# Performance work log

Hardware: AMD Instinct MI355X
Metric: run time of the kernel (lower is better)

## Reference

```python
import jax, jax.numpy as jnp
import numpy as np

H = 2048          # hidden_size
E = 8             # num_experts
TOPK = 2          # num_experts_per_tok
I = 1408          # moe_intermediate_size
IS = 5632         # shared_expert_intermediate_size


def setup_inputs() -> dict:
    key = jax.random.key(0)
    ks = jax.random.split(key, 10)
    s = 0.02
    return {
        "hidden_states": jax.random.normal(ks[0], (2, 512, H), dtype=jnp.float32),
        "gate_w": jax.random.normal(ks[1], (H, E), dtype=jnp.float32) * s,
        "wg": jax.random.normal(ks[2], (E, H, I), dtype=jnp.float32) * s,
        "wu": jax.random.normal(ks[3], (E, H, I), dtype=jnp.float32) * s,
        "wd": jax.random.normal(ks[4], (E, I, H), dtype=jnp.float32) * s,
        "sg": jax.random.normal(ks[5], (H, IS), dtype=jnp.float32) * s,
        "su": jax.random.normal(ks[6], (H, IS), dtype=jnp.float32) * s,
        "sd": jax.random.normal(ks[7], (IS, H), dtype=jnp.float32) * s,
        "shared_gate_w": jax.random.normal(ks[8], (H, 1), dtype=jnp.float32) * s,
    }


def reference(hidden_states, gate_w, wg, wu, wd, sg, su, sd, shared_gate_w):
    B, S, Hd = hidden_states.shape
    x = hidden_states.reshape(-1, Hd)                       # [T, H]
    # Router (softmax in fp32, as in the torch code)
    router_logits = x @ gate_w                              # [T, E]
    probs = jax.nn.softmax(router_logits.astype(jnp.float32), axis=-1)
    rw, sel = jax.lax.top_k(probs, TOPK)                    # [T, K]
    # norm_topk_prob = False -> no renormalization
    rw = rw.astype(x.dtype)
    # Dense combine weights: w[t,e] = sum_k rw[t,k] * 1[sel[t,k]==e]
    combine = (jax.nn.one_hot(sel, E, dtype=x.dtype) * rw[..., None]).sum(axis=1)  # [T, E]
    # Per-expert SwiGLU MLP over all tokens, zero-weighted where unselected
    g = jnp.einsum('th,ehi->eti', x, wg)                    # [E, T, I]
    u = jnp.einsum('th,ehi->eti', x, wu)                    # [E, T, I]
    y = jnp.einsum('eti,eih->eth', jax.nn.silu(g) * u, wd)  # [E, T, H]
    moe_out = jnp.einsum('eth,te->th', y, combine)          # [T, H]
    # Shared expert with sigmoid gate
    shared = (jax.nn.silu(x @ sg) * (x @ su)) @ sd          # [T, H]
    shared = jax.nn.sigmoid(x @ shared_gate_w) * shared     # [T, H]
    final = moe_out + shared
    return final.reshape(B, S, Hd), router_logits
```

## Files before the change

### kernel.cpp

```cpp
#include <hip/hip_runtime.h>
#include <cstdint>
#include <cstddef>

#define Tn 1024
#define Hn 2048
#define En 8
#define In 1408
#define ISn 5632

typedef __attribute__((ext_vector_type(8))) short bf16x8;
typedef __attribute__((ext_vector_type(4))) float f32x4;

__device__ __forceinline__ unsigned short f2bf(float f) {
  unsigned u = __builtin_bit_cast(unsigned, f);
  u += 0x7fffu + ((u >> 16) & 1u);
  return (unsigned short)(u >> 16);
}

#define PK2(a, b) ((unsigned)f2bf(a) | ((unsigned)f2bf(b) << 16))
#define SWZC(row, kc) (((kc) ^ ((row) & 7) ^ (((row) >> 3) & 7)) & 7)
#define SWZ(row, bir) (((row) << 7) | (SWZC((row), ((bir) >> 4)) << 4) | ((bir) & 15))

__global__ void router_kernel(const float* __restrict__ x, const float* __restrict__ gw,
                              const float* __restrict__ sgw, float* __restrict__ logits_out,
                              float* __restrict__ sgate, int* __restrict__ tokList,
                              float* __restrict__ wgt, int* __restrict__ cnt) {
  int t = blockIdx.x;
  int l = threadIdx.x;
  const float* xr = x + (size_t)t * Hn;
  float acc[En];
#pragma unroll
  for (int e = 0; e < En; ++e) acc[e] = 0.f;
  float accs = 0.f;
  for (int h = l; h < Hn; h += 64) {
    float xv = xr[h];
    const float4 g0 = *(const float4*)(gw + (size_t)h * En);
    const float4 g1 = *(const float4*)(gw + (size_t)h * En + 4);
    acc[0] += xv * g0.x; acc[1] += xv * g0.y; acc[2] += xv * g0.z; acc[3] += xv * g0.w;
    acc[4] += xv * g1.x; acc[5] += xv * g1.y; acc[6] += xv * g1.z; acc[7] += xv * g1.w;
    accs += xv * sgw[h];
  }
#pragma unroll
  for (int e = 0; e < En; ++e) {
#pragma unroll
    for (int off = 32; off > 0; off >>= 1) acc[e] += __shfl_down(acc[e], off);
  }
#pragma unroll
  for (int off = 32; off > 0; off >>= 1) accs += __shfl_down(accs, off);
  if (l == 0) {
    float mx = acc[0];
#pragma unroll
    for (int e = 1; e < En; ++e) mx = fmaxf(mx, acc[e]);
    float p[En], s = 0.f;
#pragma unroll
    for (int e = 0; e < En; ++e) { p[e] = expf(acc[e] - mx); s += p[e]; }
    float inv = 1.f / s;
#pragma unroll
    for (int e = 0; e < En; ++e) p[e] *= inv;
    int i1 = 0;
#pragma unroll
    for (int e = 1; e < En; ++e) if (p[e] > p[i1]) i1 = e;
    int i2 = (i1 == 0) ? 1 : 0;
#pragma unroll
    for (int e = 0; e < En; ++e) if (e != i1 && p[e] > p[i2]) i2 = e;
    int p1 = atomicAdd(&cnt[i1], 1);
    tokList[(i1 << 10) + p1] = t; wgt[(i1 << 10) + p1] = p[i1];
    int p2 = atomicAdd(&cnt[i2], 1);
    tokList[(i2 << 10) + p2] = t; wgt[(i2 << 10) + p2] = p[i2];
    sgate[t] = 1.f / (1.f + expf(-accs));
#pragma unroll
    for (int e = 0; e < En; ++e) logits_out[t * En + e] = acc[e];
  }
}

__global__ void cvt_x_kernel(const float* __restrict__ x, unsigned short* __restrict__ xb) {
  int i = (blockIdx.x * 256 + threadIdx.x) << 2;
  float4 v = *(const float4*)(x + i);
  ushort4 o;
  o.x = f2bf(v.x); o.y = f2bf(v.y); o.z = f2bf(v.z); o.w = f2bf(v.w);
  *(ushort4*)(xb + i) = o;
}

__device__ __forceinline__ void stage_b(char* sB, const float* __restrict__ src, int ldb, int tid) {
  const int kb = tid >> 5;
  const int nb = tid & 31;
  const float* p = src + (size_t)(kb * 8) * ldb + nb * 4;
  float4 r0 = *(const float4*)p; p += ldb;
  float4 r1 = *(const float4*)p; p += ldb;
  float4 r2 = *(const float4*)p; p += ldb;
  float4 r3 = *(const float4*)p; p += ldb;
  float4 r4 = *(const float4*)p; p += ldb;
  float4 r5 = *(const float4*)p; p += ldb;
  float4 r6 = *(const float4*)p; p += ldb;
  float4 r7 = *(const float4*)p;
  uint4 pk;
  int n, off;
#define STORE_ROW(J, F)                                                        \
  n = nb * 4 + (J);                                                            \
  pk.x = PK2(r0.F, r1.F); pk.y = PK2(r2.F, r3.F);                              \
  pk.z = PK2(r4.F, r5.F); pk.w = PK2(r6.F, r7.F);                              \
  off = (n << 7) | (SWZC(n, kb) << 4);                                         \
  *(uint4*)(sB + off) = pk;
  STORE_ROW(0, x)
  STORE_ROW(1, y)
  STORE_ROW(2, z)
  STORE_ROW(3, w)
#undef STORE_ROW
}

__global__ __launch_bounds__(256, 2)
void gateup_kernel(const unsigned short* __restrict__ xb,
                   const float* __restrict__ Wg, const float* __restrict__ Wu,
                   const float* __restrict__ wgt, const float* __restrict__ sgate,
                   const int* __restrict__ tokList, const int* __restrict__ cnt,
                   unsigned short* __restrict__ actout, int N, int mode) {
  const int e = blockIdx.y;
  const int nt = blockIdx.x >> 3, mt = blockIdx.x & 7;
  const int cntE = (mode == 0) ? cnt[e] : Tn;
  const int m0 = mt << 7, n0 = nt << 7;
  if (m0 >= cntE) return;

  __shared__ char smem[48 * 1024];
  char* sA = smem;
  char* sBg = smem + 16 * 1024;
  char* sBu = smem + 32 * 1024;

  const int tid = threadIdx.x;
  const int lane = tid & 63;
  const int wid = tid >> 6;
  const int wm = wid >> 1, wn = wid & 1;

  const float* Bg0 = Wg + (size_t)e * Hn * N + n0;
  const float* Bu0 = Wu + (size_t)e * Hn * N + n0;
  unsigned short* aout = actout + (size_t)e * Tn * N;

  int tokq[4];
#pragma unroll
  for (int q = 0; q < 4; ++q) {
    int row = (tid + (q << 8)) >> 3;
    int m = m0 + row;
    if (mode == 0) {
      int mc = m < cntE ? m : cntE - 1;
      tokq[q] = tokList[(e << 10) + mc];
    } else {
      tokq[q] = m;
    }
  }

  f32x4 accg[4][4], accu[4][4];
#pragma unroll
  for (int i = 0; i < 4; ++i)
#pragma unroll
    for (int j = 0; j < 4; ++j) {
      accg[i][j] = {0.f, 0.f, 0.f, 0.f};
      accu[i][j] = {0.f, 0.f, 0.f, 0.f};
    }

  for (int kt = 0; kt < Hn / 64; ++kt) {
    const int k0 = kt << 6;
#pragma unroll
    for (int q = 0; q < 4; ++q) {
      int cc = tid + (q << 8);
      int row = cc >> 3, c = cc & 7;
      uint4 v = *(const uint4*)(xb + (size_t)tokq[q] * Hn + k0 + (c << 3));
      *(uint4*)(sA + SWZ(row, c << 4)) = v;
    }
    stage_b(sBg, Bg0 + (size_t)k0 * N, N, tid);
    stage_b(sBu, Bu0 + (size_t)k0 * N, N, tid);
    __syncthreads();
#pragma unroll
    for (int kk = 0; kk < 2; ++kk) {
      bf16x8 af[4], bg[4], bu[4];
      const int bir = (kk << 6) + ((lane >> 4) << 4);
#pragma unroll
      for (int mi = 0; mi < 4; ++mi) {
        int row = (wm << 6) + (mi << 4) + (lane & 15);
        af[mi] = *(const bf16x8*)(sA + SWZ(row, bir));
      }
#pragma unroll
      for (int ni = 0; ni < 4; ++ni) {
        int n = (wn << 6) + (ni << 4) + (lane & 15);
        bg[ni] = *(const bf16x8*)(sBg + SWZ(n, bir));
        bu[ni] = *(const bf16x8*)(sBu + SWZ(n, bir));
      }
#pragma unroll
      for (int mi = 0; mi < 4; ++mi)
#pragma unroll
        for (int ni = 0; ni < 4; ++ni) {
          accg[mi][ni] = __builtin_amdgcn_mfma_f32_16x16x32_bf16(af[mi], bg[ni], accg[mi][ni], 0, 0, 0);
          accu[mi][ni] = __builtin_amdgcn_mfma_f32_16x16x32_bf16(af[mi], bu[ni], accu[mi][ni], 0, 0, 0);
        }
    }
    __syncthreads();
  }

#pragma unroll
  for (int mi = 0; mi < 4; ++mi)
#pragma unroll
    for (int ni = 0; ni < 4; ++ni)
#pragma unroll
      for (int r = 0; r < 4; ++r) {
        int m = m0 + (wm << 6) + (mi << 4) + ((lane >> 4) << 2) + r;
        int n = n0 + (wn << 6) + (ni << 4) + (lane & 15);
        if (m < cntE) {
          float sc = (mode == 0) ? wgt[(e << 10) + m] : sgate[m];
          float g = accg[mi][ni][r];
          float u = accu[mi][ni][r];
          aout[(size_t)m * N + n] = f2bf(sc * (g / (1.f + __expf(-g))) * u);
        }
      }
}

__global__ __launch_bounds__(256, 2)
void down_e_kernel(const unsigned short* __restrict__ act, const float* __restrict__ wd,
                   const int* __restrict__ tokList, const int* __restrict__ cnt,
                   float* __restrict__ out) {
  const int e = blockIdx.y;
  const int nt = blockIdx.x >> 3, mt = blockIdx.x & 7;
  const int cntE = cnt[e];
  const int m0 = mt << 7, n0 = nt << 7;
  if (m0 >= cntE) return;

  __shared__ char smem[32 * 1024];
  char* sA = smem;
  char* sB = smem + 16 * 1024;

  const int tid = threadIdx.x;
  const int lane = tid & 63;
  const int wid = tid >> 6;
  const int wm = wid >> 1, wn = wid & 1;

  const unsigned short* aBase = act + ((size_t)e * Tn + m0) * In;
  const float* bBase = wd + (size_t)e * In * Hn + n0;

  f32x4 acc[4][4];
#pragma unroll
  for (int i = 0; i < 4; ++i)
#pragma unroll
    for (int j = 0; j < 4; ++j) acc[i][j] = {0.f, 0.f, 0.f, 0.f};

  for (int kt = 0; kt < In / 64; ++kt) {
    const int k0 = kt << 6;
#pragma unroll
    for (int q = 0; q < 4; ++q) {
      int cc = tid + (q << 8);
      int row = cc >> 3, c = cc & 7;
      uint4 v = *(const uint4*)(aBase + (size_t)row * In + k0 + (c << 3));
      *(uint4*)(sA + SWZ(row, c << 4)) = v;
    }
    stage_b(sB, bBase + (size_t)k0 * Hn, Hn, tid);
    __syncthreads();
#pragma unroll
    for (int kk = 0; kk < 2; ++kk) {
      bf16x8 af[4], bf[4];
      const int bir = (kk << 6) + ((lane >> 4) << 4);
#pragma unroll
      for (int mi = 0; mi < 4; ++mi) {
        int row = (wm << 6) + (mi << 4) + (lane & 15);
        af[mi] = *(const bf16x8*)(sA + SWZ(row, bir));
      }
#pragma unroll
      for (int ni = 0; ni < 4; ++ni) {
        int n = (wn << 6) + (ni << 4) + (lane & 15);
        bf[ni] = *(const bf16x8*)(sB + SWZ(n, bir));
      }
#pragma unroll
      for (int mi = 0; mi < 4; ++mi)
#pragma unroll
        for (int ni = 0; ni < 4; ++ni)
          acc[mi][ni] = __builtin_amdgcn_mfma_f32_16x16x32_bf16(af[mi], bf[ni], acc[mi][ni], 0, 0, 0);
    }
    __syncthreads();
  }

#pragma unroll
  for (int mi = 0; mi < 4; ++mi)
#pragma unroll
    for (int ni = 0; ni < 4; ++ni)
#pragma unroll
      for (int r = 0; r < 4; ++r) {
        int m = m0 + (wm << 6) + (mi << 4) + ((lane >> 4) << 2) + r;
        int n = n0 + (wn << 6) + (ni << 4) + (lane & 15);
        if (m < cntE) {
          int tok = tokList[(e << 10) + m];
          atomicAdd(out + (size_t)tok * Hn + n, acc[mi][ni][r]);
        }
      }
}

__global__ __launch_bounds__(256, 2)
void down_s_kernel(const unsigned short* __restrict__ acts, const float* __restrict__ sd,
                   float* __restrict__ out) {
  const int nt = blockIdx.x >> 3, mt = blockIdx.x & 7;
  const int m0 = mt << 7, n0 = nt << 7;
  const int ktBeg = blockIdx.y * 44, ktEnd = ktBeg + 44;

  __shared__ char smem[32 * 1024];
  char* sA = smem;
  char* sB = smem + 16 * 1024;

  const int tid = threadIdx.x;
  const int lane = tid & 63;
  const int wid = tid >> 6;
  const int wm = wid >> 1, wn = wid & 1;

  f32x4 acc[4][4];
#pragma unroll
  for (int i = 0; i < 4; ++i)
#pragma unroll
    for (int j = 0; j < 4; ++j) acc[i][j] = {0.f, 0.f, 0.f, 0.f};

  for (int kt = ktBeg; kt < ktEnd; ++kt) {
    const int k0 = kt << 6;
#pragma unroll
    for (int q = 0; q < 4; ++q) {
      int cc = tid + (q << 8);
      int row = cc >> 3, c = cc & 7;
      uint4 v = *(const uint4*)(acts + (size_t)(m0 + row) * ISn + k0 + (c << 3));
      *(uint4*)(sA + SWZ(row, c << 4)) = v;
    }
    stage_b(sB, sd + (size_t)k0 * Hn + n0, Hn, tid);
    __syncthreads();
#pragma unroll
    for (int kk = 0; kk < 2; ++kk) {
      bf16x8 af[4], bf[4];
      const int bir = (kk << 6) + ((lane >> 4) << 4);
#pragma unroll
      for (int mi = 0; mi < 4; ++mi) {
        int row = (wm << 6) + (mi << 4) + (lane & 15);
        af[mi] = *(const bf16x8*)(sA + SWZ(row, bir));
      }
#pragma unroll
      for (int ni = 0; ni < 4; ++ni) {
        int n = (wn << 6) + (ni << 4) + (lane & 15);
        bf[ni] = *(const bf16x8*)(sB + SWZ(n, bir));
      }
#pragma unroll
      for (int mi = 0; mi < 4; ++mi)
#pragma unroll
        for (int ni = 0; ni < 4; ++ni)
          acc[mi][ni] = __builtin_amdgcn_mfma_f32_16x16x32_bf16(af[mi], bf[ni], acc[mi][ni], 0, 0, 0);
    }
    __syncthreads();
  }

#pragma unroll
  for (int mi = 0; mi < 4; ++mi)
#pragma unroll
    for (int ni = 0; ni < 4; ++ni)
#pragma unroll
      for (int r = 0; r < 4; ++r) {
        int m = m0 + (wm << 6) + (mi << 4) + ((lane >> 4) << 2) + r;
        int n = n0 + (wn << 6) + (ni << 4) + (lane & 15);
        atomicAdd(out + (size_t)m * Hn + n, acc[mi][ni][r]);
      }
}

extern "C" void kernel_launch(void* const* d_in, const int* in_sizes, int n_in,
                              void* d_out, int out_size, void* d_ws, size_t ws_size,
                              hipStream_t stream) {
  const float* x   = (const float*)d_in[0];
  const float* gw  = (const float*)d_in[1];
  const float* wg  = (const float*)d_in[2];
  const float* wu  = (const float*)d_in[3];
  const float* wd  = (const float*)d_in[4];
  const float* sg  = (const float*)d_in[5];
  const float* su  = (const float*)d_in[6];
  const float* sd  = (const float*)d_in[7];
  const float* sgw = (const float*)d_in[8];
  float* out = (float*)d_out;
  float* logits_out = out + (size_t)Tn * Hn;

  char* w = (char*)d_ws;
  int*   cnt     = (int*)w;
  float* sgate   = (float*)(w + 4096);
  int*   tokList = (int*)(w + 8192);
  float* wgt     = (float*)(w + 40960);
  unsigned short* xb   = (unsigned short*)(w + 131072);
  unsigned short* actE = xb + (size_t)Tn * Hn;
  unsigned short* actS = actE + (size_t)En * Tn * In;

  hipMemsetAsync(d_out, 0, (size_t)out_size * sizeof(float), stream);
  hipMemsetAsync(cnt, 0, En * sizeof(int), stream);
  router_kernel<<<Tn, 64, 0, stream>>>(x, gw, sgw, logits_out, sgate, tokList, wgt, cnt);
  cvt_x_kernel<<<(Tn * Hn / 4) / 256, 256, 0, stream>>>(x, xb);
  gateup_kernel<<<dim3((In / 128) * 8, En), 256, 0, stream>>>(xb, wg, wu, wgt, sgate, tokList, cnt, actE, In, 0);
  gateup_kernel<<<dim3((ISn / 128) * 8, 1), 256, 0, stream>>>(xb, sg, su, wgt, sgate, tokList, cnt, actS, ISn, 1);
  down_e_kernel<<<dim3(16 * 8, En), 256, 0, stream>>>(actE, wd, tokList, cnt, out);
  down_s_kernel<<<dim3(16 * 8, 2), 256, 0, stream>>>(actS, sd, out);
}
```

Measured before the change: 904.3 us.

## Pre-transpose weights to bf16 and stage GEMM tiles via direct global-to-LDS loads

Adds a prepass kernel that converts and transposes all expert and shared weights to bf16 K-contiguous layout every call. The GEMM kernels then fill LDS with global_load_lds 16-byte copies in swizzled order instead of loading fp32, converting, and repacking in registers. Gate/up and down launches for routed and shared experts are merged into single launches. This removes in-loop conversion and uncoalesced strided fp32 reads, but adds a full read-and-write pass over all weights each call.

```diff
diff --git a/kernel.cpp b/kernel.cpp
--- a/kernel.cpp
+++ b/kernel.cpp
@@ -11,13 +11,16 @@
 typedef __attribute__((ext_vector_type(8))) short bf16x8;
 typedef __attribute__((ext_vector_type(4))) float f32x4;
 
+typedef __attribute__((address_space(3))) unsigned int lds_u32_t;
+typedef __attribute__((address_space(1))) const unsigned int gbl_u32_t;
+#define GLL16(gp, lp) __builtin_amdgcn_global_load_lds((gbl_u32_t*)(gp), (lds_u32_t*)(lp), 16, 0, 0)
+
 __device__ __forceinline__ unsigned short f2bf(float f) {
   unsigned u = __builtin_bit_cast(unsigned, f);
   u += 0x7fffu + ((u >> 16) & 1u);
   return (unsigned short)(u >> 16);
 }
 
-#define PK2(a, b) ((unsigned)f2bf(a) | ((unsigned)f2bf(b) << 16))
 #define SWZC(row, kc) (((kc) ^ ((row) & 7) ^ (((row) >> 3) & 7)) & 7)
 #define SWZ(row, bir) (((row) << 7) | (SWZC((row), ((bir) >> 4)) << 4) | ((bir) & 15))
 
@@ -81,42 +84,80 @@
   *(ushort4*)(xb + i) = o;
 }
 
-__device__ __forceinline__ void stage_b(char* sB, const float* __restrict__ src, int ldb, int tid) {
-  const int kb = tid >> 5;
-  const int nb = tid & 31;
-  const float* p = src + (size_t)(kb * 8) * ldb + nb * 4;
-  float4 r0 = *(const float4*)p; p += ldb;
-  float4 r1 = *(const float4*)p; p += ldb;
-  float4 r2 = *(const float4*)p; p += ldb;
-  float4 r3 = *(const float4*)p; p += ldb;
-  float4 r4 = *(const float4*)p; p += ldb;
-  float4 r5 = *(const float4*)p; p += ldb;
-  float4 r6 = *(const float4*)p; p += ldb;
-  float4 r7 = *(const float4*)p;
-  uint4 pk;
-  int n, off;
-#define STORE_ROW(J, F)                                                        \
-  n = nb * 4 + (J);                                                            \
-  pk.x = PK2(r0.F, r1.F); pk.y = PK2(r2.F, r3.F);                              \
-  pk.z = PK2(r4.F, r5.F); pk.w = PK2(r6.F, r7.F);                              \
-  off = (n << 7) | (SWZC(n, kb) << 4);                                         \
-  *(uint4*)(sB + off) = pk;
-  STORE_ROW(0, x)
-  STORE_ROW(1, y)
-  STORE_ROW(2, z)
-  STORE_ROW(3, w)
-#undef STORE_ROW
+__global__ void trans_cvt_kernel(const float* __restrict__ wg, const float* __restrict__ wu,
+                                 const float* __restrict__ wd, const float* __restrict__ sg,
+                                 const float* __restrict__ su, const float* __restrict__ sd,
+                                 unsigned short* __restrict__ wgT, unsigned short* __restrict__ wuT,
+                                 unsigned short* __restrict__ wdT, unsigned short* __restrict__ sgT,
+                                 unsigned short* __restrict__ suT, unsigned short* __restrict__ sdT) {
+  __shared__ unsigned short lds[64][68];
+  const int bx = blockIdx.x, tid = threadIdx.x;
+  const float* src; unsigned short* dst; int R, C, tr, tc;
+  if (bx < 11264) {
+    int b = (bx < 5632) ? bx : bx - 5632;
+    const float* s0 = (bx < 5632) ? wg : wu;
+    unsigned short* d0 = (bx < 5632) ? wgT : wuT;
+    int e = b / 704, t = b - e * 704;
+    src = s0 + (size_t)e * Hn * In; dst = d0 + (size_t)e * In * Hn;
+    R = Hn; C = In; tr = t / 22; tc = t - tr * 22;
+  } else if (bx < 16896) {
+    int b = bx - 11264; int e = b / 704, t = b - e * 704;
+    src = wd + (size_t)e * In * Hn; dst = wdT + (size_t)e * Hn * In;
+    R = In; C = Hn; tr = t / 32; tc = t - tr * 32;
+  } else if (bx < 22528) {
+    int b = bx - 16896;
+    src = (b < 2816) ? sg : su; dst = (b < 2816) ? sgT : suT;
+    if (b >= 2816) b -= 2816;
+    R = Hn; C = ISn; tr = b / 88; tc = b - tr * 88;
+  } else {
+    int b = bx - 22528;
+    src = sd; dst = sdT; R = ISn; C = Hn; tr = b / 32; tc = b - tr * 32;
+  }
+  const int r0 = tr << 6, c0 = tc << 6;
+#pragma unroll
+  for (int q = 0; q < 4; ++q) {
+    int r = (tid >> 4) + (q << 4);
+    int c = (tid & 15) << 2;
+    float4 v = *(const float4*)(src + (size_t)(r0 + r) * C + c0 + c);
+    ushort4 o; o.x = f2bf(v.x); o.y = f2bf(v.y); o.z = f2bf(v.z); o.w = f2bf(v.w);
+    *(ushort4*)&lds[r][c] = o;
+  }
+  __syncthreads();
+  {
+    int oc = tid >> 2, ch = tid & 3;
+#pragma unroll
+    for (int g = ch; g < 8; g += 4) {
+      unsigned t0, t1, t2, t3;
+      t0 = (unsigned)lds[(g << 3) + 0][oc] | ((unsigned)lds[(g << 3) + 1][oc] << 16);
+      t1 = (unsigned)lds[(g << 3) + 2][oc] | ((unsigned)lds[(g << 3) + 3][oc] << 16);
+      t2 = (unsigned)lds[(g << 3) + 4][oc] | ((unsigned)lds[(g << 3) + 5][oc] << 16);
+      t3 = (unsigned)lds[(g << 3) + 6][oc] | ((unsigned)lds[(g << 3) + 7][oc] << 16);
+      uint4 o; o.x = t0; o.y = t1; o.z = t2; o.w = t3;
+      *(uint4*)(dst + (size_t)(c0 + oc) * R + r0 + (g << 3)) = o;
+    }
+  }
 }
 
 __global__ __launch_bounds__(256, 2)
 void gateup_kernel(const unsigned short* __restrict__ xb,
-                   const float* __restrict__ Wg, const float* __restrict__ Wu,
+                   const unsigned short* __restrict__ wgT, const unsigned short* __restrict__ wuT,
+                   const unsigned short* __restrict__ sgT, const unsigned short* __restrict__ suT,
                    const float* __restrict__ wgt, const float* __restrict__ sgate,
                    const int* __restrict__ tokList, const int* __restrict__ cnt,
-                   unsigned short* __restrict__ actout, int N, int mode) {
-  const int e = blockIdx.y;
-  const int nt = blockIdx.x >> 3, mt = blockIdx.x & 7;
-  const int cntE = (mode == 0) ? cnt[e] : Tn;
+                   unsigned short* __restrict__ actE, unsigned short* __restrict__ actS) {
+  const int bx = blockIdx.x;
+  int e, nt, mt, N, cntE, mode;
+  const unsigned short *bgp, *bup;
+  unsigned short* aout;
+  if (bx < 704) {
+    mode = 0; e = bx / 88; int r = bx - e * 88; nt = r >> 3; mt = r & 7;
+    N = In; cntE = cnt[e];
+    bgp = wgT + (size_t)e * In * Hn; bup = wuT + (size_t)e * In * Hn;
+    aout = actE + (size_t)e * Tn * In;
+  } else {
+    mode = 1; e = 0; int r = bx - 704; nt = r >> 3; mt = r & 7;
+    N = ISn; cntE = Tn; bgp = sgT; bup = suT; aout = actS;
+  }
   const int m0 = mt << 7, n0 = nt << 7;
   if (m0 >= cntE) return;
 
@@ -125,27 +166,26 @@
   char* sBg = smem + 16 * 1024;
   char* sBu = smem + 32 * 1024;
 
-  const int tid = threadIdx.x;
-  const int lane = tid & 63;
-  const int wid = tid >> 6;
+  const int tid = threadIdx.x, lane = tid & 63, wid = tid >> 6;
   const int wm = wid >> 1, wn = wid & 1;
-
-  const float* Bg0 = Wg + (size_t)e * Hn * N + n0;
-  const float* Bu0 = Wu + (size_t)e * Hn * N + n0;
-  unsigned short* aout = actout + (size_t)e * Tn * N;
-
-  int tokq[4];
+  const int qr = lane >> 3;
+  const int qc = lane & 7;
+
+  const char *gA[4], *gB[4], *gU[4];
 #pragma unroll
   for (int q = 0; q < 4; ++q) {
-    int row = (tid + (q << 8)) >> 3;
+    int row = (wid << 5) + (q << 3) + qr;
+    int chunk = SWZC(row, qc);
     int m = m0 + row;
-    if (mode == 0) {
-      int mc = m < cntE ? m : cntE - 1;
-      tokq[q] = tokList[(e << 10) + mc];
-    } else {
-      tokq[q] = m;
-    }
-  }
+    int tok;
+    if (mode == 0) { int mc = m < cntE ? m : cntE - 1; tok = tokList[(e << 10) + mc]; }
+    else tok = m;
+    gA[q] = (const char*)(xb + (size_t)tok * Hn) + chunk * 16;
+    int n = n0 + row;
+    gB[q] = (const char*)(bgp + (size_t)n * Hn) + chunk * 16;
+    gU[q] = (const char*)(bup + (size_t)n * Hn) + chunk * 16;
+  }
+  const int lbase = wid << 12;
 
   f32x4 accg[4][4], accu[4][4];
 #pragma unroll
@@ -157,16 +197,14 @@
     }
 
   for (int kt = 0; kt < Hn / 64; ++kt) {
-    const int k0 = kt << 6;
+    const int koff = kt << 7;
 #pragma unroll
     for (int q = 0; q < 4; ++q) {
-      int cc = tid + (q << 8);
-      int row = cc >> 3, c = cc & 7;
-      uint4 v = *(const uint4*)(xb + (size_t)tokq[q] * Hn + k0 + (c << 3));
-      *(uint4*)(sA + SWZ(row, c << 4)) = v;
-    }
-    stage_b(sBg, Bg0 + (size_t)k0 * N, N, tid);
-    stage_b(sBu, Bu0 + (size_t)k0 * N, N, tid);
+      GLL16(gA[q] + koff, sA + lbase + (q << 10));
+      GLL16(gB[q] + koff, sBg + lbase + (q << 10));
+      GLL16(gU[q] + koff, sBu + lbase + (q << 10));
+    }
+    asm volatile("s_waitcnt vmcnt(0)" ::: "memory");
     __syncthreads();
 #pragma unroll
     for (int kk = 0; kk < 2; ++kk) {
@@ -212,26 +250,46 @@
 }
 
 __global__ __launch_bounds__(256, 2)
-void down_e_kernel(const unsigned short* __restrict__ act, const float* __restrict__ wd,
-                   const int* __restrict__ tokList, const int* __restrict__ cnt,
-                   float* __restrict__ out) {
-  const int e = blockIdx.y;
-  const int nt = blockIdx.x >> 3, mt = blockIdx.x & 7;
-  const int cntE = cnt[e];
+void down_kernel(const unsigned short* __restrict__ actE, const unsigned short* __restrict__ actS,
+                 const unsigned short* __restrict__ wdT, const unsigned short* __restrict__ sdT,
+                 const int* __restrict__ tokList, const int* __restrict__ cnt,
+                 float* __restrict__ out) {
+  const int bx = blockIdx.x;
+  int e, nt, mt, cntE, mode, ktBeg, ktEnd, ldk;
+  const unsigned short *aBase, *bBase;
+  if (bx < 1024) {
+    mode = 0; e = bx >> 7; int r = bx & 127; nt = r >> 3; mt = r & 7;
+    cntE = cnt[e];
+    if ((mt << 7) >= cntE) return;
+    ldk = In; ktBeg = 0; ktEnd = In / 64;
+    aBase = actE + (size_t)e * Tn * In + (size_t)(mt << 7) * In;
+    bBase = wdT + (size_t)e * Hn * In + (size_t)(nt << 7) * In;
+  } else {
+    mode = 1; e = 0; int bs = bx - 1024; int split = bs >> 7; int r = bs & 127;
+    nt = r >> 3; mt = r & 7; cntE = Tn;
+    ldk = ISn; ktBeg = split * 44; ktEnd = ktBeg + 44;
+    aBase = actS + (size_t)(mt << 7) * ISn;
+    bBase = sdT + (size_t)(nt << 7) * ISn;
+  }
   const int m0 = mt << 7, n0 = nt << 7;
-  if (m0 >= cntE) return;
 
   __shared__ char smem[32 * 1024];
   char* sA = smem;
   char* sB = smem + 16 * 1024;
 
-  const int tid = threadIdx.x;
-  const int lane = tid & 63;
-  const int wid = tid >> 6;
+  const int tid = threadIdx.x, lane = tid & 63, wid = tid >> 6;
   const int wm = wid >> 1, wn = wid & 1;
-
-  const unsigned short* aBase = act + ((size_t)e * Tn + m0) * In;
-  const float* bBase = wd + (size_t)e * In * Hn + n0;
+  const int qr = lane >> 3, qc = lane & 7;
+
+  const char *gA[4], *gB[4];
+#pragma unroll
+  for (int q = 0; q < 4; ++q) {
+    int row = (wid << 5) + (q << 3) + qr;
+    int chunk = SWZC(row, qc);
+    gA[q] = (const char*)(aBase + (size_t)row * ldk) + chunk * 16;
+    gB[q] = (const char*)(bBase + (size_t)row * ldk) + chunk * 16;
+  }
+  const int lbase = wid << 12;
 
   f32x4 acc[4][4];
 #pragma unroll
@@ -239,16 +297,14 @@
 #pragma unroll
     for (int j = 0; j < 4; ++j) acc[i][j] = {0.f, 0.f, 0.f, 0.f};
 
-  for (int kt = 0; kt < In / 64; ++kt) {
-    const int k0 = kt << 6;
+  for (int kt = ktBeg; kt < ktEnd; ++kt) {
+    const int koff = kt << 7;
 #pragma unroll
     for (int q = 0; q < 4; ++q) {
-      int cc = tid + (q << 8);
-      int row = cc >> 3, c = cc & 7;
-      uint4 v = *(const uint4*)(aBase + (size_t)row * In + k0 + (c << 3));
-      *(uint4*)(sA + SWZ(row, c << 4)) = v;
-    }
-    stage_b(sB, bBase + (size_t)k0 * Hn, Hn, tid);
+      GLL16(gA[q] + koff, sA + lbase + (q << 10));
+      GLL16(gB[q] + koff, sB + lbase + (q << 10));
+    }
+    asm volatile("s_waitcnt vmcnt(0)" ::: "memory");
     __syncthreads();
 #pragma unroll
     for (int kk = 0; kk < 2; ++kk) {
@@ -281,78 +337,14 @@
       for (int r = 0; r < 4; ++r) {
         int m = m0 + (wm << 6) + (mi << 4) + ((lane >> 4) << 2) + r;
         int n = n0 + (wn << 6) + (ni << 4) + (lane & 15);
-        if (m < cntE) {
-          int tok = tokList[(e << 10) + m];
-          atomicAdd(out + (size_t)tok * Hn + n, acc[mi][ni][r]);
+        if (mode == 0) {
+          if (m < cntE) {
+            int tok = tokList[(e << 10) + m];
+            atomicAdd(out + (size_t)tok * Hn + n, acc[mi][ni][r]);
+          }
+        } else {
+          atomicAdd(out + (size_t)m * Hn + n, acc[mi][ni][r]);
         }
-      }
-}
-
-__global__ __launch_bounds__(256, 2)
-void down_s_kernel(const unsigned short* __restrict__ acts, const float* __restrict__ sd,
-                   float* __restrict__ out) {
-  const int nt = blockIdx.x >> 3, mt = blockIdx.x & 7;
-  const int m0 = mt << 7, n0 = nt << 7;
-  const int ktBeg = blockIdx.y * 44, ktEnd = ktBeg + 44;
-
-  __shared__ char smem[32 * 1024];
-  char* sA = smem;
-  char* sB = smem + 16 * 1024;
-
-  const int tid = threadIdx.x;
-  const int lane = tid & 63;
-  const int wid = tid >> 6;
-  const int wm = wid >> 1, wn = wid & 1;
-
-  f32x4 acc[4][4];
-#pragma unroll
-  for (int i = 0; i < 4; ++i)
-#pragma unroll
-    for (int j = 0; j < 4; ++j) acc[i][j] = {0.f, 0.f, 0.f, 0.f};
-
-  for (int kt = ktBeg; kt < ktEnd; ++kt) {
-    const int k0 = kt << 6;
-#pragma unroll
-    for (int q = 0; q < 4; ++q) {
-      int cc = tid + (q << 8);
-      int row = cc >> 3, c = cc & 7;
-      uint4 v = *(const uint4*)(acts + (size_t)(m0 + row) * ISn + k0 + (c << 3));
-      *(uint4*)(sA + SWZ(row, c << 4)) = v;
-    }
-    stage_b(sB, sd + (size_t)k0 * Hn + n0, Hn, tid);
-    __syncthreads();
-#pragma unroll
-    for (int kk = 0; kk < 2; ++kk) {
-      bf16x8 af[4], bf[4];
-      const int bir = (kk << 6) + ((lane >> 4) << 4);
-#pragma unroll
-      for (int mi = 0; mi < 4; ++mi) {
-        int row = (wm << 6) + (mi << 4) + (lane & 15);
-        af[mi] = *(const bf16x8*)(sA + SWZ(row, bir));
-      }
-#pragma unroll
-      for (int ni = 0; ni < 4; ++ni) {
-        int n = (wn << 6) + (ni << 4) + (lane & 15);
-        bf[ni] = *(const bf16x8*)(sB + SWZ(n, bir));
-      }
-#pragma unroll
-      for (int mi = 0; mi < 4; ++mi)
-#pragma unroll
-        for (int ni = 0; ni < 4; ++ni)
-          acc[mi][ni] = __builtin_amdgcn_mfma_f32_16x16x32_bf16(af[mi], bf[ni], acc[mi][ni], 0, 0, 0);
-    }
-    __syncthreads();
-  }
-
-#pragma unroll
-  for (int mi = 0; mi < 4; ++mi)
-#pragma unroll
-    for (int ni = 0; ni < 4; ++ni)
-#pragma unroll
-      for (int r = 0; r < 4; ++r) {
-        int m = m0 + (wm << 6) + (mi << 4) + ((lane >> 4) << 2) + r;
-        int n = n0 + (wn << 6) + (ni << 4) + (lane & 15);
-        atomicAdd(out + (size_t)m * Hn + n, acc[mi][ni][r]);
       }
 }
 
@@ -376,16 +368,22 @@
   float* sgate   = (float*)(w + 4096);
   int*   tokList = (int*)(w + 8192);
   float* wgt     = (float*)(w + 40960);
-  unsigned short* xb   = (unsigned short*)(w + 131072);
+  unsigned short* u = (unsigned short*)(w + 131072);
+  unsigned short* xb   = u;
   unsigned short* actE = xb + (size_t)Tn * Hn;
   unsigned short* actS = actE + (size_t)En * Tn * In;
+  unsigned short* wgT  = actS + (size_t)Tn * ISn;
+  unsigned short* wuT  = wgT + (size_t)En * In * Hn;
+  unsigned short* wdT  = wuT + (size_t)En * In * Hn;
+  unsigned short* sgT  = wdT + (size_t)En * Hn * In;
+  unsigned short* suT  = sgT + (size_t)ISn * Hn;
+  unsigned short* sdT  = suT + (size_t)ISn * Hn;
 
   hipMemsetAsync(d_out, 0, (size_t)out_size * sizeof(float), stream);
   hipMemsetAsync(cnt, 0, En * sizeof(int), stream);
   router_kernel<<<Tn, 64, 0, stream>>>(x, gw, sgw, logits_out, sgate, tokList, wgt, cnt);
   cvt_x_kernel<<<(Tn * Hn / 4) / 256, 256, 0, stream>>>(x, xb);
-  gateup_kernel<<<dim3((In / 128) * 8, En), 256, 0, stream>>>(xb, wg, wu, wgt, sgate, tokList, cnt, actE, In, 0);
-  gateup_kernel<<<dim3((ISn / 128) * 8, 1), 256, 0, stream>>>(xb, sg, su, wgt, sgate, tokList, cnt, actS, ISn, 1);
-  down_e_kernel<<<dim3(16 * 8, En), 256, 0, stream>>>(actE, wd, tokList, cnt, out);
-  down_s_kernel<<<dim3(16 * 8, 2), 256, 0, stream>>>(actS, sd, out);
-}
+  trans_cvt_kernel<<<25344, 256, 0, stream>>>(wg, wu, wd, sg, su, sd, wgT, wuT, wdT, sgT, suT, sdT);
+  gateup_kernel<<<704 + 352, 256, 0, stream>>>(xb, wgT, wuT, sgT, suT, wgt, sgate, tokList, cnt, actE, actS);
+  down_kernel<<<1024 + 256, 256, 0, stream>>>(actE, actS, wdT, sdT, tokList, cnt, out);
+}
```

Result: faster. 780.7 us (-13.7%).
